# Kernel tuning notes

Hardware: AMD Instinct MI355X
Metric: run time of the kernel (lower is better)

## Reference

```python
import jax, jax.numpy as jnp
import numpy as np

N_PIXELS = 1024 * 1024      # flattened image W*H
N_CLASSES = 100             # logit channels / label vocabulary
N_SEGMENTS = 30             # superpixel_regions


def setup_inputs() -> dict:
    key = jax.random.key(0)
    k1, k2, k3 = jax.random.split(key, 3)
    output = jax.random.normal(k1, (N_PIXELS, N_CLASSES), dtype=jnp.float32)
    target = jax.random.randint(k2, (N_PIXELS,), 0, N_CLASSES, dtype=jnp.int64)
    seg_ids = jax.random.randint(k3, (N_PIXELS,), 0, N_SEGMENTS, dtype=jnp.int32)
    return {"output": output, "target": target, "seg_ids": seg_ids}


def reference(output, target, seg_ids):
    # --- per-superpixel histogram mode-voting relabel ---
    # counts[s, c] = number of pixels in superpixel s currently labeled c.
    counts = jnp.zeros((N_SEGMENTS, N_CLASSES), dtype=jnp.int32)
    counts = counts.at[seg_ids, target].add(1)
    # np.argmax over hist of np.unique-sorted labels == smallest class id among ties,
    # which jnp.argmax over the dense class axis reproduces exactly.
    mode = jnp.argmax(counts, axis=1)              # [S]
    relabeled = mode[seg_ids].astype(target.dtype)  # [N]

    # --- CrossEntropyLoss(output, target): mean NLL of log-softmax ---
    logp = jax.nn.log_softmax(output, axis=-1)                       # [N, C]
    nll = -jnp.take_along_axis(logp, target[:, None], axis=-1)[:, 0]  # [N]
    loss = jnp.mean(nll)
    return loss, relabeled
```

## Files before the change

kernel.cpp:

```cpp
#include <hip/hip_runtime.h>
#include <math.h>

#define NCLASS 100
#define NSEG 30
#define NREP 8
#define F4_PER_ROW 25
#define ROWS_PER_GRP 16
#define F4_PER_GRP (F4_PER_ROW * ROWS_PER_GRP)

__device__ __forceinline__ float e4(float4 v) {
    return __expf(v.x) + __expf(v.y) + __expf(v.z) + __expf(v.w);
}

__global__ __launch_bounds__(256) void ce_hist_kernel(
    const float* __restrict__ logits,
    const int*   __restrict__ target,
    const int*   __restrict__ seg,
    int N,
    int*    __restrict__ g_counts,
    double* __restrict__ g_loss)
{
    __shared__ int    lds_hist[NSEG * NCLASS];
    __shared__ float  part[4][F4_PER_GRP];
    __shared__ double lds_loss[4];

    for (int i = threadIdx.x; i < NSEG * NCLASS; i += blockDim.x) lds_hist[i] = 0;
    __syncthreads();

    const int lane          = threadIdx.x & 63;
    const int wv            = threadIdx.x >> 6;
    const int sub           = lane & 3;
    const int q             = lane >> 2;
    const int wavesPerBlock = blockDim.x >> 6;
    const int gwave         = blockIdx.x * wavesPerBlock + wv;
    const int totWaves      = gridDim.x * wavesPerBlock;
    const int ngroups       = N >> 4;

    double acc = 0.0;

    for (int grp = gwave; grp < ngroups; grp += totWaves) {
        const int row = grp * ROWS_PER_GRP + q;

        const int t = target[row];
        const int s = seg[row];

        const float4* g4 = (const float4*)logits + (size_t)grp * F4_PER_GRP;
        float4 f0 = g4[lane        ];
        float4 f1 = g4[lane + 64   ];
        float4 f2 = g4[lane + 128  ];
        float4 f3 = g4[lane + 192  ];
        float4 f4v= g4[lane + 256  ];
        float4 f5 = g4[lane + 320  ];

        part[wv][lane      ] = e4(f0);
        part[wv][lane + 64 ] = e4(f1);
        part[wv][lane + 128] = e4(f2);
        part[wv][lane + 192] = e4(f3);
        part[wv][lane + 256] = e4(f4v);
        part[wv][lane + 320] = e4(f5);
        if (lane < 16) {
            float4 f6 = g4[lane + 384];
            part[wv][lane + 384] = e4(f6);
        }

        const int base = F4_PER_ROW * q + sub;
        float e = part[wv][base     ] + part[wv][base + 4 ] + part[wv][base + 8 ]
                + part[wv][base + 12] + part[wv][base + 16] + part[wv][base + 20];
        if (sub == 0) e += part[wv][F4_PER_ROW * q + 24];
        e += __shfl_xor(e, 1);
        e += __shfl_xor(e, 2);

        const float xt = logits[(size_t)row * NCLASS + t];

        if (sub == 0) {
            acc += (double)(__logf(e) - xt);
            atomicAdd(&lds_hist[s * NCLASS + t], 1);
        }
    }

    #pragma unroll
    for (int off = 32; off; off >>= 1) acc += __shfl_xor(acc, off);
    if (lane == 0) lds_loss[wv] = acc;
    __syncthreads();

    if (threadIdx.x == 0) {
        double b = 0.0;
        for (int w = 0; w < wavesPerBlock; ++w) b += lds_loss[w];
        atomicAdd(g_loss, b);
    }
    int* my_counts = g_counts + (blockIdx.x & (NREP - 1)) * (NSEG * NCLASS);
    for (int i = threadIdx.x; i < NSEG * NCLASS; i += blockDim.x) {
        int c = lds_hist[i];
        if (c) atomicAdd(&my_counts[i], c);
    }
}

__global__ void finalize_kernel(
    const int* __restrict__ g_counts,
    const double* __restrict__ g_loss,
    int N,
    int* __restrict__ g_mode,
    float* __restrict__ out_loss)
{
    const int t = threadIdx.x;
    const int s = t >> 3;
    const int j = t & 7;
    if (s < NSEG) {
        int bestKey = -1;
        for (int c = j; c < NCLASS; c += 8) {
            int v = 0;
            #pragma unroll
            for (int r = 0; r < NREP; ++r)
                v += g_counts[r * (NSEG * NCLASS) + s * NCLASS + c];
            int key = (v << 7) | (127 - c);
            bestKey = max(bestKey, key);
        }
        bestKey = max(bestKey, __shfl_xor(bestKey, 1));
        bestKey = max(bestKey, __shfl_xor(bestKey, 2));
        bestKey = max(bestKey, __shfl_xor(bestKey, 4));
        if (j == 0) g_mode[s] = 127 - (bestKey & 127);
    }
    if (t == 0) out_loss[0] = (float)(g_loss[0] / (double)N);
}

__global__ __launch_bounds__(256) void relabel_kernel(
    const int* __restrict__ seg,
    const int* __restrict__ g_mode,
    float* __restrict__ out,
    int N)
{
    __shared__ float mode_f[NSEG];
    for (int i = threadIdx.x; i < NSEG; i += blockDim.x)
        mode_f[i] = (float)g_mode[i];
    __syncthreads();

    int idx    = blockIdx.x * blockDim.x + threadIdx.x;
    int stride = gridDim.x * blockDim.x;
    for (int i = idx; i < N; i += stride)
        out[i] = mode_f[seg[i]];
}

extern "C" void kernel_launch(void* const* d_in, const int* in_sizes, int n_in,
                              void* d_out, int out_size, void* d_ws, size_t ws_size,
                              hipStream_t stream)
{
    const float* logits = (const float*)d_in[0];
    const int*   target = (const int*)d_in[1];
    const int*   seg    = (const int*)d_in[2];
    float* out = (float*)d_out;

    const int N = in_sizes[1];

    double* g_loss   = (double*)d_ws;
    int*    g_counts = (int*)((char*)d_ws + 16);
    int*    g_mode   = (int*)((char*)d_ws + 16 + (size_t)NREP * NSEG * NCLASS * sizeof(int));

    hipMemsetAsync(d_ws, 0, 16 + (size_t)NREP * NSEG * NCLASS * sizeof(int), stream);

    ce_hist_kernel<<<1024, 256, 0, stream>>>(logits, target, seg, N, g_counts, g_loss);
    finalize_kernel<<<1, 256, 0, stream>>>(g_counts, g_loss, N, g_mode, out);
    relabel_kernel<<<2048, 256, 0, stream>>>(seg, g_mode, out + 1, N);
}
```

Before: 99.74 us.

## Replace global histogram atomics with per-block private 16-bit histograms and parallel finalize

Each CE block now writes its LDS histogram, packed as 16-bit counts, and its partial loss to private workspace slots instead of doing global atomics. This also removes the workspace memset. A 31-block finalize kernel sums the 1024 partial histograms per segment and the loss partials. The aim is to avoid contended atomics and the memset launch, at the cost of extra global traffic (about 6 MB written and read back) and a slower serial reduction loop in finalize. A fallback to the old atomic path is kept for when the workspace is too small.

Measured after the change: 100.5 us. About the same (+0.8%).

```diff
diff --git a/kernel.cpp b/kernel.cpp
--- a/kernel.cpp
+++ b/kernel.cpp
@@ -3,10 +3,12 @@
 
 #define NCLASS 100
 #define NSEG 30
+#define HBINS (NSEG * NCLASS)
 #define NREP 8
 #define F4_PER_ROW 25
 #define ROWS_PER_GRP 16
 #define F4_PER_GRP (F4_PER_ROW * ROWS_PER_GRP)
+#define CE_BLOCKS 1024
 
 __device__ __forceinline__ float e4(float4 v) {
     return __expf(v.x) + __expf(v.y) + __expf(v.z) + __expf(v.w);
@@ -17,14 +19,15 @@
     const int*   __restrict__ target,
     const int*   __restrict__ seg,
     int N,
-    int*    __restrict__ g_counts,
-    double* __restrict__ g_loss)
-{
-    __shared__ int    lds_hist[NSEG * NCLASS];
+    void*   __restrict__ flush_dst,
+    double* __restrict__ loss_dst,
+    int priv)
+{
+    __shared__ int    lds_hist[HBINS];
     __shared__ float  part[4][F4_PER_GRP];
     __shared__ double lds_loss[4];
 
-    for (int i = threadIdx.x; i < NSEG * NCLASS; i += blockDim.x) lds_hist[i] = 0;
+    for (int i = threadIdx.x; i < HBINS; i += blockDim.x) lds_hist[i] = 0;
     __syncthreads();
 
     const int lane          = threadIdx.x & 63;
@@ -83,19 +86,79 @@
     if (lane == 0) lds_loss[wv] = acc;
     __syncthreads();
 
-    if (threadIdx.x == 0) {
-        double b = 0.0;
-        for (int w = 0; w < wavesPerBlock; ++w) b += lds_loss[w];
-        atomicAdd(g_loss, b);
-    }
-    int* my_counts = g_counts + (blockIdx.x & (NREP - 1)) * (NSEG * NCLASS);
-    for (int i = threadIdx.x; i < NSEG * NCLASS; i += blockDim.x) {
-        int c = lds_hist[i];
-        if (c) atomicAdd(&my_counts[i], c);
-    }
-}
-
-__global__ void finalize_kernel(
+    if (priv) {
+        if (threadIdx.x == 0) {
+            double b = 0.0;
+            for (int w = 0; w < wavesPerBlock; ++w) b += lds_loss[w];
+            loss_dst[blockIdx.x] = b;
+        }
+        unsigned int* my = (unsigned int*)flush_dst + (size_t)blockIdx.x * (HBINS / 2);
+        for (int i = threadIdx.x; i < HBINS / 2; i += blockDim.x) {
+            unsigned int u = (unsigned int)lds_hist[2 * i]
+                           | ((unsigned int)lds_hist[2 * i + 1] << 16);
+            my[i] = u;
+        }
+    } else {
+        if (threadIdx.x == 0) {
+            double b = 0.0;
+            for (int w = 0; w < wavesPerBlock; ++w) b += lds_loss[w];
+            atomicAdd(loss_dst, b);
+        }
+        int* my = (int*)flush_dst + (size_t)(blockIdx.x & (NREP - 1)) * HBINS;
+        for (int i = threadIdx.x; i < HBINS; i += blockDim.x) {
+            int c = lds_hist[i];
+            if (c) atomicAdd(&my[i], c);
+        }
+    }
+}
+
+__global__ __launch_bounds__(256) void finalize_priv_kernel(
+    const unsigned short* __restrict__ counts,
+    const double* __restrict__ loss_part,
+    int N,
+    int* __restrict__ g_mode,
+    float* __restrict__ out_loss)
+{
+    __shared__ int    tot2[2][NCLASS];
+    __shared__ double ls[4];
+
+    const int b = blockIdx.x;
+    if (b < NSEG) {
+        const int c    = threadIdx.x & 127;
+        const int half = threadIdx.x >> 7;
+        int v = 0;
+        if (c < NCLASS) {
+            const unsigned short* base =
+                counts + (size_t)half * (CE_BLOCKS / 2) * HBINS + b * NCLASS + c;
+            for (int r = 0; r < CE_BLOCKS / 2; ++r)
+                v += base[(size_t)r * HBINS];
+            tot2[half][c] = v;
+        }
+        __syncthreads();
+        if (threadIdx.x < 64) {
+            int bestKey = -1;
+            for (int c2 = threadIdx.x; c2 < NCLASS; c2 += 64) {
+                int key = ((tot2[0][c2] + tot2[1][c2]) << 7) | (127 - c2);
+                bestKey = max(bestKey, key);
+            }
+            #pragma unroll
+            for (int off = 32; off; off >>= 1)
+                bestKey = max(bestKey, __shfl_xor(bestKey, off));
+            if (threadIdx.x == 0) g_mode[b] = 127 - (bestKey & 127);
+        }
+    } else {
+        double v = 0.0;
+        for (int i = threadIdx.x; i < CE_BLOCKS; i += blockDim.x) v += loss_part[i];
+        #pragma unroll
+        for (int off = 32; off; off >>= 1) v += __shfl_xor(v, off);
+        if ((threadIdx.x & 63) == 0) ls[threadIdx.x >> 6] = v;
+        __syncthreads();
+        if (threadIdx.x == 0)
+            out_loss[0] = (float)((ls[0] + ls[1] + ls[2] + ls[3]) / (double)N);
+    }
+}
+
+__global__ void finalize_fallback_kernel(
     const int* __restrict__ g_counts,
     const double* __restrict__ g_loss,
     int N,
@@ -111,7 +174,7 @@
             int v = 0;
             #pragma unroll
             for (int r = 0; r < NREP; ++r)
-                v += g_counts[r * (NSEG * NCLASS) + s * NCLASS + c];
+                v += g_counts[r * HBINS + s * NCLASS + c];
             int key = (v << 7) | (127 - c);
             bestKey = max(bestKey, key);
         }
@@ -151,13 +214,30 @@
 
     const int N = in_sizes[1];
 
-    double* g_loss   = (double*)d_ws;
-    int*    g_counts = (int*)((char*)d_ws + 16);
-    int*    g_mode   = (int*)((char*)d_ws + 16 + (size_t)NREP * NSEG * NCLASS * sizeof(int));
-
-    hipMemsetAsync(d_ws, 0, 16 + (size_t)NREP * NSEG * NCLASS * sizeof(int), stream);
-
-    ce_hist_kernel<<<1024, 256, 0, stream>>>(logits, target, seg, N, g_counts, g_loss);
-    finalize_kernel<<<1, 256, 0, stream>>>(g_counts, g_loss, N, g_mode, out);
-    relabel_kernel<<<2048, 256, 0, stream>>>(seg, g_mode, out + 1, N);
-}
+    const size_t loss_bytes   = (size_t)CE_BLOCKS * sizeof(double);
+    const size_t counts_bytes = (size_t)CE_BLOCKS * HBINS * sizeof(unsigned short);
+    const size_t need_priv    = loss_bytes + counts_bytes + 256;
+
+    if (ws_size >= need_priv) {
+        double*         loss_part = (double*)d_ws;
+        unsigned short* counts    = (unsigned short*)((char*)d_ws + loss_bytes);
+        int*            g_mode    = (int*)((char*)d_ws + loss_bytes + counts_bytes);
+
+        ce_hist_kernel<<<CE_BLOCKS, 256, 0, stream>>>(
+            logits, target, seg, N, (void*)counts, loss_part, 1);
+        finalize_priv_kernel<<<NSEG + 1, 256, 0, stream>>>(
+            counts, loss_part, N, g_mode, out);
+        relabel_kernel<<<2048, 256, 0, stream>>>(seg, g_mode, out + 1, N);
+    } else {
+        double* g_loss   = (double*)d_ws;
+        int*    g_counts = (int*)((char*)d_ws + 16);
+        int*    g_mode   = (int*)((char*)d_ws + 16 + (size_t)NREP * HBINS * sizeof(int));
+
+        hipMemsetAsync(d_ws, 0, 16 + (size_t)NREP * HBINS * sizeof(int), stream);
+        ce_hist_kernel<<<CE_BLOCKS, 256, 0, stream>>>(
+            logits, target, seg, N, (void*)g_counts, g_loss, 0);
+        finalize_fallback_kernel<<<1, 256, 0, stream>>>(
+            g_counts, g_loss, N, g_mode, out);
+        relabel_kernel<<<2048, 256, 0, stream>>>(seg, g_mode, out + 1, N);
+    }
+}
```

## Split histogram pass, fuse relabel into cross-entropy pass with ticket-based loss finalize

Applied to the files above, without the earlier changes.

Moves the segment/class histogram into its own lightweight kernel that reads only target and seg as int4. Each block writes a private 16-bit packed histogram, which removes the memset and the global atomics. A multi-block finalize computes the per-segment modes and resets the loss and ticket. The relabel write is then fused into the cross-entropy pass, and the last block to take a ticket writes the mean loss, which removes the separate relabel kernel and its second read of seg. The trade-off is an extra pass over target and seg before the large logits pass, plus a dependency on workspace size.

Result: slower. 140.9 us (+41.3%).

```diff
diff --git a/kernel.cpp b/kernel.cpp
--- a/kernel.cpp
+++ b/kernel.cpp
@@ -3,7 +3,10 @@
 
 #define NCLASS 100
 #define NSEG 30
+#define HBINS (NSEG * NCLASS)
+#define HIST_BLOCKS 512
 #define NREP 8
+#define CE_BLOCKS 1024
 #define F4_PER_ROW 25
 #define ROWS_PER_GRP 16
 #define F4_PER_GRP (F4_PER_ROW * ROWS_PER_GRP)
@@ -12,19 +15,103 @@
     return __expf(v.x) + __expf(v.y) + __expf(v.z) + __expf(v.w);
 }
 
-__global__ __launch_bounds__(256) void ce_hist_kernel(
+__global__ __launch_bounds__(256) void hist_kernel(
+    const int* __restrict__ target,
+    const int* __restrict__ seg,
+    int N,
+    void* __restrict__ dst,
+    int priv)
+{
+    __shared__ int h[HBINS];
+    for (int i = threadIdx.x; i < HBINS; i += blockDim.x) h[i] = 0;
+    __syncthreads();
+
+    const int4* t4 = (const int4*)target;
+    const int4* s4 = (const int4*)seg;
+    const int i4PerBlock = (N / 4) / gridDim.x;
+    const int base = blockIdx.x * i4PerBlock;
+    for (int k = threadIdx.x; k < i4PerBlock; k += blockDim.x) {
+        int4 t = t4[base + k];
+        int4 s = s4[base + k];
+        atomicAdd(&h[s.x * NCLASS + t.x], 1);
+        atomicAdd(&h[s.y * NCLASS + t.y], 1);
+        atomicAdd(&h[s.z * NCLASS + t.z], 1);
+        atomicAdd(&h[s.w * NCLASS + t.w], 1);
+    }
+    __syncthreads();
+
+    if (priv) {
+        unsigned int* my = (unsigned int*)dst + (size_t)blockIdx.x * (HBINS / 2);
+        for (int i = threadIdx.x; i < HBINS / 2; i += blockDim.x)
+            my[i] = (unsigned int)h[2 * i] | ((unsigned int)h[2 * i + 1] << 16);
+    } else {
+        int* my = (int*)dst + (size_t)(blockIdx.x & (NREP - 1)) * HBINS;
+        for (int i = threadIdx.x; i < HBINS; i += blockDim.x) {
+            int c = h[i];
+            if (c) atomicAdd(&my[i], c);
+        }
+    }
+}
+
+__global__ __launch_bounds__(256) void finalize_kernel(
+    const void* __restrict__ counts,
+    int priv,
+    int* __restrict__ g_mode,
+    double* __restrict__ g_loss,
+    int* __restrict__ g_ticket)
+{
+    __shared__ int tot2[2][NCLASS];
+    const int b = blockIdx.x;
+    if (b < NSEG) {
+        const int c    = threadIdx.x & 127;
+        const int half = threadIdx.x >> 7;
+        if (c < NCLASS) {
+            int v = 0;
+            if (priv) {
+                const unsigned short* p = (const unsigned short*)counts
+                    + (size_t)half * (HIST_BLOCKS / 2) * HBINS + b * NCLASS + c;
+                for (int r = 0; r < HIST_BLOCKS / 2; ++r)
+                    v += p[(size_t)r * HBINS];
+            } else if (half == 0) {
+                #pragma unroll
+                for (int r = 0; r < NREP; ++r)
+                    v += ((const int*)counts)[r * HBINS + b * NCLASS + c];
+            }
+            tot2[half][c] = v;
+        }
+        __syncthreads();
+        if (threadIdx.x < 64) {
+            int bestKey = -1;
+            for (int c2 = threadIdx.x; c2 < NCLASS; c2 += 64) {
+                int key = ((tot2[0][c2] + tot2[1][c2]) << 7) | (127 - c2);
+                bestKey = max(bestKey, key);
+            }
+            #pragma unroll
+            for (int off = 32; off; off >>= 1)
+                bestKey = max(bestKey, __shfl_xor(bestKey, off));
+            if (threadIdx.x == 0) g_mode[b] = 127 - (bestKey & 127);
+        }
+    } else if (threadIdx.x == 0) {
+        *g_loss = 0.0;
+        *g_ticket = 0;
+    }
+}
+
+__global__ __launch_bounds__(256) void ce_relabel_kernel(
     const float* __restrict__ logits,
     const int*   __restrict__ target,
     const int*   __restrict__ seg,
     int N,
-    int*    __restrict__ g_counts,
-    double* __restrict__ g_loss)
-{
-    __shared__ int    lds_hist[NSEG * NCLASS];
+    const int* __restrict__ g_mode,
+    double* __restrict__ g_loss,
+    int*    __restrict__ g_ticket,
+    float*  __restrict__ out)
+{
     __shared__ float  part[4][F4_PER_GRP];
     __shared__ double lds_loss[4];
-
-    for (int i = threadIdx.x; i < NSEG * NCLASS; i += blockDim.x) lds_hist[i] = 0;
+    __shared__ float  mode_f[NSEG];
+
+    if (threadIdx.x < NSEG) mode_f[threadIdx.x] = (float)g_mode[threadIdx.x];
     __syncthreads();
 
     const int lane          = threadIdx.x & 63;
@@ -74,7 +161,7 @@
 
         if (sub == 0) {
             acc += (double)(__logf(e) - xt);
-            atomicAdd(&lds_hist[s * NCLASS + t], 1);
+            out[1 + row] = mode_f[s];
         }
     }
 
@@ -87,57 +174,13 @@
         double b = 0.0;
         for (int w = 0; w < wavesPerBlock; ++w) b += lds_loss[w];
         atomicAdd(g_loss, b);
-    }
-    int* my_counts = g_counts + (blockIdx.x & (NREP - 1)) * (NSEG * NCLASS);
-    for (int i = threadIdx.x; i < NSEG * NCLASS; i += blockDim.x) {
-        int c = lds_hist[i];
-        if (c) atomicAdd(&my_counts[i], c);
-    }
-}
-
-__global__ void finalize_kernel(
-    const int* __restrict__ g_counts,
-    const double* __restrict__ g_loss,
-    int N,
-    int* __restrict__ g_mode,
-    float* __restrict__ out_loss)
-{
-    const int t = threadIdx.x;
-    const int s = t >> 3;
-    const int j = t & 7;
-    if (s < NSEG) {
-        int bestKey = -1;
-        for (int c = j; c < NCLASS; c += 8) {
-            int v = 0;
-            #pragma unroll
-            for (int r = 0; r < NREP; ++r)
-                v += g_counts[r * (NSEG * NCLASS) + s * NCLASS + c];
-            int key = (v << 7) | (127 - c);
-            bestKey = max(bestKey, key);
-        }
-        bestKey = max(bestKey, __shfl_xor(bestKey, 1));
-        bestKey = max(bestKey, __shfl_xor(bestKey, 2));
-        bestKey = max(bestKey, __shfl_xor(bestKey, 4));
-        if (j == 0) g_mode[s] = 127 - (bestKey & 127);
-    }
-    if (t == 0) out_loss[0] = (float)(g_loss[0] / (double)N);
-}
-
-__global__ __launch_bounds__(256) void relabel_kernel(
-    const int* __restrict__ seg,
-    const int* __restrict__ g_mode,
-    float* __restrict__ out,
-    int N)
-{
-    __shared__ float mode_f[NSEG];
-    for (int i = threadIdx.x; i < NSEG; i += blockDim.x)
-        mode_f[i] = (float)g_mode[i];
-    __syncthreads();
-
-    int idx    = blockIdx.x * blockDim.x + threadIdx.x;
-    int stride = gridDim.x * blockDim.x;
-    for (int i = idx; i < N; i += stride)
-        out[i] = mode_f[seg[i]];
+        __threadfence();
+        int done = atomicAdd(g_ticket, 1);
+        if (done == (int)gridDim.x - 1) {
+            double tot = atomicAdd(g_loss, 0.0);
+            out[0] = (float)(tot / (double)N);
+        }
+    }
 }
 
 extern "C" void kernel_launch(void* const* d_in, const int* in_sizes, int n_in,
@@ -151,13 +194,29 @@
 
     const int N = in_sizes[1];
 
-    double* g_loss   = (double*)d_ws;
-    int*    g_counts = (int*)((char*)d_ws + 16);
-    int*    g_mode   = (int*)((char*)d_ws + 16 + (size_t)NREP * NSEG * NCLASS * sizeof(int));
-
-    hipMemsetAsync(d_ws, 0, 16 + (size_t)NREP * NSEG * NCLASS * sizeof(int), stream);
-
-    ce_hist_kernel<<<1024, 256, 0, stream>>>(logits, target, seg, N, g_counts, g_loss);
-    finalize_kernel<<<1, 256, 0, stream>>>(g_counts, g_loss, N, g_mode, out);
-    relabel_kernel<<<2048, 256, 0, stream>>>(seg, g_mode, out + 1, N);
-}
+    const size_t priv_counts_bytes = (size_t)HIST_BLOCKS * HBINS * sizeof(unsigned short);
+    const size_t fb_counts_bytes   = (size_t)NREP * HBINS * sizeof(int);
+
+    if (ws_size >= priv_counts_bytes + 256) {
+        void*   counts   = d_ws;
+        int*    g_mode   = (int*)((char*)d_ws + priv_counts_bytes);
+        double* g_loss   = (double*)((char*)d_ws + priv_counts_bytes + 128);
+        int*    g_ticket = (int*)((char*)d_ws + priv_counts_bytes + 136);
+
+        hist_kernel<<<HIST_BLOCKS, 256, 0, stream>>>(target, seg, N, counts, 1);
+        finalize_kernel<<<NSEG + 1, 256, 0, stream>>>(counts, 1, g_mode, g_loss, g_ticket);
+        ce_relabel_kernel<<<CE_BLOCKS, 256, 0, stream>>>(
+            logits, target, seg, N, g_mode, g_loss, g_ticket, out);
+    } else {
+        void*   counts   = d_ws;
+        int*    g_mode   = (int*)((char*)d_ws + fb_counts_bytes);
+        double* g_loss   = (double*)((char*)d_ws + fb_counts_bytes + 128);
+        int*    g_ticket = (int*)((char*)d_ws + fb_counts_bytes + 136);
+
+        hipMemsetAsync(counts, 0, fb_counts_bytes, stream);
+        hist_kernel<<<HIST_BLOCKS, 256, 0, stream>>>(target, seg, N, counts, 0);
+        finalize_kernel<<<NSEG + 1, 256, 0, stream>>>(counts, 0, g_mode, g_loss, g_ticket);
+        ce_relabel_kernel<<<CE_BLOCKS, 256, 0, stream>>>(
+            logits, target, seg, N, g_mode, g_loss, g_ticket, out);
+    }
+}
```
